# Performance work log

Measured on AMD Instinct MI355X. Metric: run time of the kernel, lower is better.

## Reference

```python
import jax, jax.numpy as jnp
import numpy as np

N = 30000      # nodes
NNZ = 480000   # edges (avg degree 16)
D_IN, D_H, D_OUT = 64, 256, 128


def spmm(rows, cols, vals, feat, n):
    # (sparse [n,n] in COO) @ feat : out[r] += vals[e] * feat[cols[e]]
    return jax.ops.segment_sum(vals[:, None] * feat[cols], rows, num_segments=n)


def graph_inception(l_feat, r_feat, rows, cols, vals, W1, b1, W2, b2):
    # hop=1, eval mode (F.dropout with training=False is identity)
    n = l_feat.shape[0]
    x0 = r_feat  # dropout(Korder_list[r][0])
    x1 = l_feat  # dropout(Korder_list[l][0])
    # network_l @ x0 and network_r (=transpose) @ x1
    l_K = spmm(rows, cols, vals, x0, n)          # [N, D]
    r_K = spmm(cols, rows, vals, x1, n)          # [N, D]
    l_re = l_K @ W1 + b1                          # weight1(l_Korder)
    r_re = r_K @ W1 + b1
    # Multiply: mm(network, a) * b then weight2 (mm result equals l_K / r_K)
    l_mul = (l_K * x1) @ W2 + b2
    r_mul = (r_K * x0) @ W2 + b2
    return l_re + l_mul, r_re + r_mul


def setup_inputs() -> dict:
    key = jax.random.key(0)
    ks = jax.random.split(key, 9)
    l_feat = jax.random.normal(ks[0], (N, D_IN), jnp.float32)
    r_feat = jax.random.normal(ks[1], (N, D_IN), jnp.float32)
    edge_rows = jax.random.randint(ks[2], (NNZ,), 0, N, jnp.int32)
    edge_cols = jax.random.randint(ks[3], (NNZ,), 0, N, jnp.int32)
    edge_vals = jax.random.uniform(ks[4], (NNZ,), jnp.float32)
    W1 = jax.random.normal(ks[5], (D_IN, D_H), jnp.float32) / np.sqrt(D_IN)
    W2 = jax.random.normal(ks[6], (D_IN, D_H), jnp.float32) / np.sqrt(D_IN)
    W3 = jax.random.normal(ks[7], (D_H, D_OUT), jnp.float32) / np.sqrt(D_H)
    W4 = jax.random.normal(ks[8], (D_H, D_OUT), jnp.float32) / np.sqrt(D_H)
    return {
        "l_feat": l_feat, "r_feat": r_feat,
        "edge_rows": edge_rows, "edge_cols": edge_cols, "edge_vals": edge_vals,
        "W1": W1, "b1": jnp.zeros((D_H,), jnp.float32),
        "W2": W2, "b2": jnp.zeros((D_H,), jnp.float32),
        "W3": W3, "b3": jnp.zeros((D_OUT,), jnp.float32),
        "W4": W4, "b4": jnp.zeros((D_OUT,), jnp.float32),
    }


def reference(l_feat, r_feat, edge_rows, edge_cols, edge_vals,
              W1, b1, W2, b2, W3, b3, W4, b4):
    a1, b1_ = graph_inception(l_feat, r_feat, edge_rows, edge_cols, edge_vals, W1, b1, W2, b2)
    y1 = jax.nn.relu(a1)
    z1 = jax.nn.relu(b1_)
    a2, _ = graph_inception(y1, z1, edge_rows, edge_cols, edge_vals, W3, b3, W4, b4)
    return jax.nn.relu(a2)  # [N, 128]
```

## Files before the change

kernel.cpp:

```cpp
#include <hip/hip_runtime.h>

#define NN     30000
#define NNZE   480000
#define NPART  8
#define PROWS  (NN / NPART)
#define NCHUNK 32
#define CH_E   (NNZE / NCHUNK)
#define HBIN   (NN / 2)
#define SCB    118

using s8 = __attribute__((ext_vector_type(8))) short;
using f4 = __attribute__((ext_vector_type(4))) float;

__device__ __forceinline__ unsigned short f2bf(float x) {
    unsigned int u = __float_as_uint(x);
    u += 0x7fff + ((u >> 16) & 1);
    return (unsigned short)(u >> 16);
}
__device__ __forceinline__ float bf2f(unsigned short h) {
    return __uint_as_float(((unsigned int)h) << 16);
}
__device__ __forceinline__ float bflo(unsigned int z) {
    return __uint_as_float(z << 16);
}
__device__ __forceinline__ float bfhi(unsigned int z) {
    return __uint_as_float(z & 0xffff0000u);
}
__device__ __forceinline__ int2 nt_pair(const int2* p) {
    long long v = __builtin_nontemporal_load((const long long*)p);
    int2 r; r.x = (int)(unsigned int)v; r.y = (int)(v >> 32); return r;
}

#define FEAT4   (NN * 64 / 4)
#define PREP_W0 (2 * FEAT4)
#define PREP_W1 (PREP_W0 + 98688)
__global__ __launch_bounds__(256) void prep_kernel(
    const float* __restrict__ lf, const float* __restrict__ rf,
    const float* __restrict__ W1, const float* __restrict__ W2,
    const float* __restrict__ W3, const float* __restrict__ W4,
    const float* __restrict__ b1, const float* __restrict__ b2,
    const float* __restrict__ b3, const float* __restrict__ b4,
    unsigned short* __restrict__ lfb, unsigned short* __restrict__ rfb,
    unsigned short* __restrict__ Wt1, unsigned short* __restrict__ Wt2,
    float* __restrict__ bias1, float* __restrict__ bias2)
{
    int i = blockIdx.x * 256 + threadIdx.x;
    if (i < PREP_W0) {
        const float* src = (i < FEAT4) ? lf : rf;
        unsigned short* dst = (i < FEAT4) ? lfb : rfb;
        int j = (i < FEAT4) ? i : i - FEAT4;
        float4 v = ((const float4*)src)[j];
        ushort4 o;
        o.x = f2bf(v.x); o.y = f2bf(v.y); o.z = f2bf(v.z); o.w = f2bf(v.w);
        ((ushort4*)dst)[j] = o;
    } else if (i < PREP_W1) {
        int j = i - PREP_W0;
        if (j < 32768) {
            int n = j >> 7, k = j & 127;
            float v = (k < 64) ? W1[(size_t)k * 256 + n] : W2[(size_t)(k - 64) * 256 + n];
            Wt1[j] = f2bf(v);
        } else if (j < 32768 + 65536) {
            int q = j - 32768;
            int n = q >> 9, k = q & 511;
            float v = (k < 256) ? W3[(size_t)k * 128 + n] : W4[(size_t)(k - 256) * 128 + n];
            Wt2[q] = f2bf(v);
        } else if (j < 98304 + 256) {
            int n = j - 98304; bias1[n] = b1[n] + b2[n];
        } else if (j < 98560 + 128) {
            int n = j - 98560; bias2[n] = b3[n] + b4[n];
        }
    }
}

__global__ __launch_bounds__(256) void count_rank_kernel(
    const int* __restrict__ rows, const int* __restrict__ cols,
    int* __restrict__ histP,
    unsigned short* __restrict__ rank_r, unsigned short* __restrict__ rank_c)
{
    int b = blockIdx.x;
    int side  = b >> 6;
    int chunk = (b & 63) >> 1;
    int half  = b & 1;
    const int* keys = side ? cols : rows;
    unsigned short* rank = side ? rank_c : rank_r;
    int binlo = half * HBIN;

    __shared__ int h[HBIN];
    for (int i = threadIdx.x; i < HBIN; i += 256) h[i] = 0;
    __syncthreads();

    int e0 = chunk * CH_E;
    for (int e = e0 + threadIdx.x; e < e0 + CH_E; e += 256) {
        int k = __builtin_nontemporal_load(keys + e) - binlo;
        if ((unsigned)k < (unsigned)HBIN)
            rank[e] = (unsigned short)atomicAdd(&h[k], 1);
    }
    __syncthreads();

    int* dst = histP + ((size_t)(side * NCHUNK + chunk)) * NN + binlo;
    for (int i = threadIdx.x; i < HBIN; i += 256)
        __builtin_nontemporal_store(h[i], dst + i);
}

__global__ __launch_bounds__(256) void scanP_kernel(
    int* __restrict__ histP,
    int* __restrict__ rp, int* __restrict__ cp, int* __restrict__ totals)
{
    int b = blockIdx.x;
    int side = (b >= SCB) ? 1 : 0;
    int lb = side ? b - SCB : b;
    int t = threadIdx.x;
    int bin = lb * 256 + t;

    int run = 0;
    if (bin < NN) {
        int* base = histP + (size_t)side * NCHUNK * NN + bin;
#pragma unroll 4
        for (int c = 0; c < NCHUNK; ++c) {
            int v = base[(size_t)c * NN];
            base[(size_t)c * NN] = run;
            run += v;
        }
    }
    __shared__ int s[256];
    s[t] = run;
    __syncthreads();
#pragma unroll
    for (int off = 1; off < 256; off <<= 1) {
        int u = (t >= off) ? s[t - off] : 0;
        __syncthreads();
        s[t] += u;
        __syncthreads();
    }
    if (bin < NN) (side ? cp : rp)[bin] = s[t] - run;
    if (t == 255) totals[b] = s[t];
}

__global__ __launch_bounds__(256) void scan_addtot_kernel(
    int* __restrict__ rp, int* __restrict__ cp, const int* __restrict__ totals)
{
    int b = blockIdx.x;
    int side = (b >= SCB) ? 1 : 0;
    int lb = side ? b - SCB : b;
    int t = threadIdx.x;

    __shared__ int s[128];
    if (t < 128) s[t] = (t < SCB) ? totals[side * SCB + t] : 0;
    __syncthreads();
#pragma unroll
    for (int off = 1; off < 128; off <<= 1) {
        int u = 0;
        if (t < 128 && t >= off) u = s[t - off];
        __syncthreads();
        if (t < 128) s[t] += u;
        __syncthreads();
    }
    int off = (lb == 0) ? 0 : s[lb - 1];
    int idx = lb * 256 + t;
    int* ptr = side ? cp : rp;
    if (idx < NN) ptr[idx] += off;
    if (b == 0   && t == 0) rp[NN] = NNZE;
    if (b == SCB && t == 0) cp[NN] = NNZE;
}

__global__ __launch_bounds__(256) void scatter_rank_kernel(
    const int* __restrict__ rows, const int* __restrict__ cols,
    const float* __restrict__ vals,
    const unsigned short* __restrict__ rank_r, const unsigned short* __restrict__ rank_c,
    const int* __restrict__ histP,
    const int* __restrict__ rp, const int* __restrict__ cp,
    int2* __restrict__ csr_pair, int2* __restrict__ csc_pair)
{
    int part = blockIdx.x & (NPART - 1);
    int lo = part * PROWS, hi = lo + PROWS;
    int nb = gridDim.x >> 3;
    int bj = blockIdx.x >> 3;
    int stride = nb * 256;
    for (int e = bj * 256 + threadIdx.x; e < NNZE; e += stride) {
        int r = __builtin_nontemporal_load(rows + e);
        int c = __builtin_nontemporal_load(cols + e);
        float fv = __builtin_nontemporal_load(vals + e);
        int vb = __float_as_int(fv);
        int chunk = e / CH_E;
        if (r >= lo && r < hi) {
            int p = rp[r] + histP[(size_t)chunk * NN + r]
                  + (int)__builtin_nontemporal_load(rank_r + e);
            csr_pair[p] = make_int2(c, vb);
        }
        if (c >= lo && c < hi) {
            int q = cp[c] + histP[(size_t)(NCHUNK + chunk) * NN + c]
                  + (int)__builtin_nontemporal_load(rank_c + e);
            csc_pair[q] = make_int2(r, vb);
        }
    }
}

__global__ __launch_bounds__(256) void gather64_x_kernel(
    const int* __restrict__ rp, const int2* __restrict__ rpair,
    const int* __restrict__ cp, const int2* __restrict__ cpair,
    const unsigned short* __restrict__ lfb, const unsigned short* __restrict__ rfb,
    unsigned short* __restrict__ X1, unsigned short* __restrict__ X2)
{
    int side = blockIdx.y;
    const int*  ptr  = side ? cp    : rp;
    const int2* pair = side ? cpair : rpair;
    const unsigned int* gf = (const unsigned int*)(side ? lfb : rfb);
    const unsigned int* mf = (const unsigned int*)(side ? rfb : lfb);
    unsigned int* X = (unsigned int*)(side ? X2 : X1);

    int w = blockIdx.x * 8 + (threadIdx.x >> 5);
    int l = threadIdx.x & 31;
    int e0 = ptr[w], e1 = ptr[w + 1];
    float a0 = 0.f, a1 = 0.f;
    int e = e0;
    for (; e + 7 < e1; e += 8) {
        int2 p[8];
#pragma unroll
        for (int j = 0; j < 8; ++j) p[j] = nt_pair(&pair[e + j]);
        unsigned int z[8];
#pragma unroll
        for (int j = 0; j < 8; ++j) z[j] = gf[(size_t)p[j].x * 32 + l];
#pragma unroll
        for (int j = 0; j < 8; ++j) {
            float v = __int_as_float(p[j].y);
            a0 += v * bflo(z[j]);
            a1 += v * bfhi(z[j]);
        }
    }
    for (; e < e1; ++e) {
        int2 p0 = nt_pair(&pair[e]);
        unsigned int z0 = gf[(size_t)p0.x * 32 + l];
        float v = __int_as_float(p0.y);
        a0 += v * bflo(z0);
        a1 += v * bfhi(z0);
    }
    unsigned int m = mf[(size_t)w * 32 + l];
    float m0 = a0 * bflo(m);
    float m1 = a1 * bfhi(m);
    X[(size_t)w * 64 + l]      = (unsigned int)f2bf(a0) | ((unsigned int)f2bf(a1) << 16);
    X[(size_t)w * 64 + 32 + l] = (unsigned int)f2bf(m0) | ((unsigned int)f2bf(m1) << 16);
}

__global__ __launch_bounds__(256) void gather256_x_kernel(
    const int* __restrict__ ptr, const int2* __restrict__ pair,
    const unsigned short* __restrict__ z1b, const unsigned short* __restrict__ y1b,
    unsigned short* __restrict__ X3)
{
    int w    = blockIdx.x * 4 + (threadIdx.x >> 6);
    int lane = threadIdx.x & 63;
    int e0 = ptr[w], e1 = ptr[w + 1];
    const ushort4* Z = (const ushort4*)z1b;
    f4 acc = {0.f, 0.f, 0.f, 0.f};
    int e = e0;
    for (; e + 7 < e1; e += 8) {
        int2 p[8];
#pragma unroll
        for (int j = 0; j < 8; ++j) p[j] = nt_pair(&pair[e + j]);
        ushort4 z[8];
#pragma unroll
        for (int j = 0; j < 8; ++j) z[j] = Z[(size_t)p[j].x * 64 + lane];
#pragma unroll
        for (int j = 0; j < 8; ++j) {
            float v = __int_as_float(p[j].y);
            acc[0] += v * bf2f(z[j].x);
            acc[1] += v * bf2f(z[j].y);
            acc[2] += v * bf2f(z[j].z);
            acc[3] += v * bf2f(z[j].w);
        }
    }
    for (; e < e1; ++e) {
        int2 p0 = nt_pair(&pair[e]);
        float v0 = __int_as_float(p0.y);
        ushort4 z0 = Z[(size_t)p0.x * 64 + lane];
        acc[0] += v0 * bf2f(z0.x);
        acc[1] += v0 * bf2f(z0.y);
        acc[2] += v0 * bf2f(z0.z);
        acc[3] += v0 * bf2f(z0.w);
    }
    ushort4 y = ((const ushort4*)y1b)[(size_t)w * 64 + lane];
    ushort4 o0, o1;
    o0.x = f2bf(acc[0]); o0.y = f2bf(acc[1]); o0.z = f2bf(acc[2]); o0.w = f2bf(acc[3]);
    o1.x = f2bf(acc[0] * bf2f(y.x));
    o1.y = f2bf(acc[1] * bf2f(y.y));
    o1.z = f2bf(acc[2] * bf2f(y.z));
    o1.w = f2bf(acc[3] * bf2f(y.w));
    ((ushort4*)X3)[(size_t)w * 128 + lane]      = o0;
    ((ushort4*)X3)[(size_t)w * 128 + 64 + lane] = o1;
}

template<int K, int DOUT, bool OUT_BF16>
__global__ __launch_bounds__(256) void mfma_gemm_kernel(
    const unsigned short* Xa, const unsigned short* Xb,
    const unsigned short* __restrict__ Wt, const float* __restrict__ bias,
    void* outa, void* outb)
{
    constexpr int WC = DOUT / 4;
    constexpr int FN = WC / 16;
    __shared__ s8 sX[64 * 8];
    __shared__ s8 sW[DOUT * 8];

    const unsigned short* X = blockIdx.y ? Xb : Xa;
    void* outv              = blockIdx.y ? outb : outa;

    const int t       = threadIdx.x;
    const int rowbase = blockIdx.x * 64;
    const int wid     = t >> 6;
    const int lane    = t & 63;
    const int l15     = lane & 15;
    const int kg      = lane >> 4;

    f4 acc[4][FN] = {};

    for (int kc = 0; kc < K; kc += 64) {
#pragma unroll
        for (int it = 0; it < 2; ++it) {
            int ch = t + it * 256;
            int r = ch >> 3, c = ch & 7;
            int row = rowbase + r;
            s8 v = {};
            if (row < NN) v = ((const s8*)X)[((size_t)row * K + kc) / 8 + c];
            sX[(r << 3) | (c ^ (r & 7))] = v;
        }
#pragma unroll
        for (int it = 0; it < DOUT / 32; ++it) {
            int ch = t + it * 256;
            int n = ch >> 3, c = ch & 7;
            sW[(n << 3) | (c ^ (n & 7))] = ((const s8*)Wt)[((size_t)n * K + kc) / 8 + c];
        }
        __syncthreads();

#pragma unroll
        for (int ks = 0; ks < 2; ++ks) {
            int cch = ks * 4 + kg;
            s8 a[4], b[FN];
#pragma unroll
            for (int fm = 0; fm < 4; ++fm) {
                int r0 = fm * 16 + l15;
                a[fm] = sX[(r0 << 3) | (cch ^ (r0 & 7))];
            }
#pragma unroll
            for (int fn = 0; fn < FN; ++fn) {
                int n0 = wid * WC + fn * 16 + l15;
                b[fn] = sW[(n0 << 3) | (cch ^ (n0 & 7))];
            }
#pragma unroll
            for (int fm = 0; fm < 4; ++fm)
#pragma unroll
                for (int fn = 0; fn < FN; ++fn)
                    acc[fm][fn] = __builtin_amdgcn_mfma_f32_16x16x32_bf16(
                        a[fm], b[fn], acc[fm][fn], 0, 0, 0);
        }
        __syncthreads();
    }

#pragma unroll
    for (int fm = 0; fm < 4; ++fm) {
#pragma unroll
        for (int fn = 0; fn < FN; ++fn) {
            int col = wid * WC + fn * 16 + l15;
            float bv = bias[col];
#pragma unroll
            for (int j = 0; j < 4; ++j) {
                int row = rowbase + fm * 16 + kg * 4 + j;
                if (row < NN) {
                    float v = fmaxf(acc[fm][fn][j] + bv, 0.f);
                    if constexpr (OUT_BF16)
                        ((unsigned short*)outv)[(size_t)row * DOUT + col] = f2bf(v);
                    else
                        ((float*)outv)[(size_t)row * DOUT + col] = v;
                }
            }
        }
    }
}

extern "C" void kernel_launch(void* const* d_in, const int* in_sizes, int n_in,
                              void* d_out, int out_size, void* d_ws, size_t ws_size,
                              hipStream_t stream)
{
    const float* l_feat = (const float*)d_in[0];
    const float* r_feat = (const float*)d_in[1];
    const int*   rows   = (const int*)  d_in[2];
    const int*   cols   = (const int*)  d_in[3];
    const float* vals   = (const float*)d_in[4];
    const float* W1     = (const float*)d_in[5];
    const float* b1     = (const float*)d_in[6];
    const float* W2     = (const float*)d_in[7];
    const float* b2     = (const float*)d_in[8];
    const float* W3     = (const float*)d_in[9];
    const float* b3     = (const float*)d_in[10];
    const float* W4     = (const float*)d_in[11];
    const float* b4     = (const float*)d_in[12];
    float* out = (float*)d_out;

    char* p = (char*)d_ws;
    unsigned short* X1  = (unsigned short*)p; p += (size_t)NN * 128 * 2;
    unsigned short* X2  = (unsigned short*)p; p += (size_t)NN * 128 * 2;
    unsigned short* X3  = (unsigned short*)p; p += (size_t)NN * 512 * 2;
    unsigned short* z1b = (unsigned short*)p; p += (size_t)NN * 256 * 2;
    unsigned short* y1b = (unsigned short*)p; p += (size_t)NN * 256 * 2;
    unsigned short* lfb = (unsigned short*)p; p += (size_t)NN * 64 * 2;
    unsigned short* rfb = (unsigned short*)p; p += (size_t)NN * 64 * 2;
    int* histP    = (int*)p; p += (size_t)2 * NCHUNK * NN * 4;
    int* totals   = (int*)p; p += 256 * 4;
    unsigned short* Wt1 = (unsigned short*)p; p += 32768 * 2;
    unsigned short* Wt2 = (unsigned short*)p; p += 65536 * 2;
    float* bias1 = (float*)p; p += 256 * 4;
    float* bias2 = (float*)p; p += 128 * 4;
    int*   row_ptr  = (int*)p; p += (size_t)(NN + 4) * 4;
    int*   col_ptr  = (int*)p; p += (size_t)(NN + 4) * 4;
    int2*  csr_pair = (int2*)p; p += (size_t)NNZE * 8;
    int2*  csc_pair = (int2*)p; p += (size_t)NNZE * 8;
    unsigned short* rank_r = (unsigned short*)p; p += (size_t)NNZE * 2;
    unsigned short* rank_c = (unsigned short*)p; p += (size_t)NNZE * 2;

    prep_kernel<<<(PREP_W1 + 255) / 256, 256, 0, stream>>>(
        l_feat, r_feat, W1, W2, W3, W4, b1, b2, b3, b4,
        lfb, rfb, Wt1, Wt2, bias1, bias2);

    count_rank_kernel<<<128, 256, 0, stream>>>(rows, cols, histP, rank_r, rank_c);

    scanP_kernel<<<2 * SCB, 256, 0, stream>>>(histP, row_ptr, col_ptr, totals);
    scan_addtot_kernel<<<2 * SCB, 256, 0, stream>>>(row_ptr, col_ptr, totals);

    scatter_rank_kernel<<<1024, 256, 0, stream>>>(
        rows, cols, vals, rank_r, rank_c, histP, row_ptr, col_ptr, csr_pair, csc_pair);

    {
        dim3 grid(NN / 8, 2);
        gather64_x_kernel<<<grid, 256, 0, stream>>>(
            row_ptr, csr_pair, col_ptr, csc_pair, lfb, rfb, X1, X2);
    }

    {
        dim3 grid((NN + 63) / 64, 2);
        mfma_gemm_kernel<128, 256, true><<<grid, 256, 0, stream>>>(
            X1, X2, Wt1, bias1, y1b, z1b);
    }

    gather256_x_kernel<<<NN / 4, 256, 0, stream>>>(row_ptr, csr_pair, z1b, y1b, X3);

    {
        dim3 grid((NN + 63) / 64, 1);
        mfma_gemm_kernel<512, 128, false><<<grid, 256, 0, stream>>>(
            X3, X3, Wt2, bias2, out, out);
    }
}
```

Before: 198.5 us.

## Stage edge pairs in LDS per block and use nontemporal loads/stores in gathers and GEMMs

Each gather block now loads its whole contiguous edge-pair range into shared memory cooperatively before per-row accumulation, so rows read their pairs from LDS instead of each warp issuing its own global loads. If a block's range exceeds the LDS capacity, the remaining pairs fall back to global loads. The gather64 unroll drops from 8 to 4. Nontemporal loads and stores are added for the gather outputs, for GEMM input tiles, and selectively for GEMM outputs, so streaming data does not evict the feature tables used by the random gathers. The trade-off is an added block-wide sync and less memory-level parallelism in gather64.

Result: no change. 199.4 us (+0.5%).

```diff
diff --git a/kernel.cpp b/kernel.cpp
--- a/kernel.cpp
+++ b/kernel.cpp
@@ -29,6 +29,9 @@
 __device__ __forceinline__ int2 nt_pair(const int2* p) {
     long long v = __builtin_nontemporal_load((const long long*)p);
     int2 r; r.x = (int)(unsigned int)v; r.y = (int)(v >> 32); return r;
+}
+__device__ __forceinline__ unsigned long long nt_u64(const void* p) {
+    return __builtin_nontemporal_load((const unsigned long long*)p);
 }
 
 #define FEAT4   (NN * 64 / 4)
@@ -195,6 +198,7 @@
     }
 }
 
+#define G64CAP 768
 __global__ __launch_bounds__(256) void gather64_x_kernel(
     const int* __restrict__ rp, const int2* __restrict__ rpair,
     const int* __restrict__ cp, const int2* __restrict__ cpair,
@@ -208,27 +212,36 @@
     const unsigned int* mf = (const unsigned int*)(side ? rfb : lfb);
     unsigned int* X = (unsigned int*)(side ? X2 : X1);
 
-    int w = blockIdx.x * 8 + (threadIdx.x >> 5);
+    __shared__ int2 sp[G64CAP];
+    int w0 = blockIdx.x * 8;
+    int e0b = ptr[w0];
+    int nseg = ptr[w0 + 8] - e0b;
+    for (int i = threadIdx.x; i < nseg && i < G64CAP; i += 256)
+        sp[i] = nt_pair(&pair[e0b + i]);
+    __syncthreads();
+
+    int w = w0 + (threadIdx.x >> 5);
     int l = threadIdx.x & 31;
-    int e0 = ptr[w], e1 = ptr[w + 1];
+    int ea = ptr[w] - e0b, eb = ptr[w + 1] - e0b;
     float a0 = 0.f, a1 = 0.f;
-    int e = e0;
-    for (; e + 7 < e1; e += 8) {
-        int2 p[8];
-#pragma unroll
-        for (int j = 0; j < 8; ++j) p[j] = nt_pair(&pair[e + j]);
-        unsigned int z[8];
-#pragma unroll
-        for (int j = 0; j < 8; ++j) z[j] = gf[(size_t)p[j].x * 32 + l];
-#pragma unroll
-        for (int j = 0; j < 8; ++j) {
+    int e = ea;
+    for (; e + 3 < eb; e += 4) {
+        int2 p[4];
+#pragma unroll
+        for (int j = 0; j < 4; ++j)
+            p[j] = (e + j < G64CAP) ? sp[e + j] : nt_pair(&pair[e0b + e + j]);
+        unsigned int z[4];
+#pragma unroll
+        for (int j = 0; j < 4; ++j) z[j] = gf[(size_t)p[j].x * 32 + l];
+#pragma unroll
+        for (int j = 0; j < 4; ++j) {
             float v = __int_as_float(p[j].y);
             a0 += v * bflo(z[j]);
             a1 += v * bfhi(z[j]);
         }
     }
-    for (; e < e1; ++e) {
-        int2 p0 = nt_pair(&pair[e]);
+    for (; e < eb; ++e) {
+        int2 p0 = (e < G64CAP) ? sp[e] : nt_pair(&pair[e0b + e]);
         unsigned int z0 = gf[(size_t)p0.x * 32 + l];
         float v = __int_as_float(p0.y);
         a0 += v * bflo(z0);
@@ -237,25 +250,37 @@
     unsigned int m = mf[(size_t)w * 32 + l];
     float m0 = a0 * bflo(m);
     float m1 = a1 * bfhi(m);
-    X[(size_t)w * 64 + l]      = (unsigned int)f2bf(a0) | ((unsigned int)f2bf(a1) << 16);
-    X[(size_t)w * 64 + 32 + l] = (unsigned int)f2bf(m0) | ((unsigned int)f2bf(m1) << 16);
-}
-
+    unsigned int o0 = (unsigned int)f2bf(a0) | ((unsigned int)f2bf(a1) << 16);
+    unsigned int o1 = (unsigned int)f2bf(m0) | ((unsigned int)f2bf(m1) << 16);
+    __builtin_nontemporal_store(o0, &X[(size_t)w * 64 + l]);
+    __builtin_nontemporal_store(o1, &X[(size_t)w * 64 + 32 + l]);
+}
+
+#define G256CAP 512
 __global__ __launch_bounds__(256) void gather256_x_kernel(
     const int* __restrict__ ptr, const int2* __restrict__ pair,
     const unsigned short* __restrict__ z1b, const unsigned short* __restrict__ y1b,
     unsigned short* __restrict__ X3)
 {
-    int w    = blockIdx.x * 4 + (threadIdx.x >> 6);
+    __shared__ int2 sp[G256CAP];
+    int w0 = blockIdx.x * 4;
+    int e0b = ptr[w0];
+    int nseg = ptr[w0 + 4] - e0b;
+    for (int i = threadIdx.x; i < nseg && i < G256CAP; i += 256)
+        sp[i] = nt_pair(&pair[e0b + i]);
+    __syncthreads();
+
+    int w    = w0 + (threadIdx.x >> 6);
     int lane = threadIdx.x & 63;
-    int e0 = ptr[w], e1 = ptr[w + 1];
+    int ea = ptr[w] - e0b, eb = ptr[w + 1] - e0b;
     const ushort4* Z = (const ushort4*)z1b;
     f4 acc = {0.f, 0.f, 0.f, 0.f};
-    int e = e0;
-    for (; e + 7 < e1; e += 8) {
+    int e = ea;
+    for (; e + 7 < eb; e += 8) {
         int2 p[8];
 #pragma unroll
-        for (int j = 0; j < 8; ++j) p[j] = nt_pair(&pair[e + j]);
+        for (int j = 0; j < 8; ++j)
+            p[j] = (e + j < G256CAP) ? sp[e + j] : nt_pair(&pair[e0b + e + j]);
         ushort4 z[8];
 #pragma unroll
         for (int j = 0; j < 8; ++j) z[j] = Z[(size_t)p[j].x * 64 + lane];
@@ -268,8 +293,8 @@
             acc[3] += v * bf2f(z[j].w);
         }
     }
-    for (; e < e1; ++e) {
-        int2 p0 = nt_pair(&pair[e]);
+    for (; e < eb; ++e) {
+        int2 p0 = (e < G256CAP) ? sp[e] : nt_pair(&pair[e0b + e]);
         float v0 = __int_as_float(p0.y);
         ushort4 z0 = Z[(size_t)p0.x * 64 + lane];
         acc[0] += v0 * bf2f(z0.x);
@@ -277,18 +302,27 @@
         acc[2] += v0 * bf2f(z0.z);
         acc[3] += v0 * bf2f(z0.w);
     }
-    ushort4 y = ((const ushort4*)y1b)[(size_t)w * 64 + lane];
-    ushort4 o0, o1;
-    o0.x = f2bf(acc[0]); o0.y = f2bf(acc[1]); o0.z = f2bf(acc[2]); o0.w = f2bf(acc[3]);
-    o1.x = f2bf(acc[0] * bf2f(y.x));
-    o1.y = f2bf(acc[1] * bf2f(y.y));
-    o1.z = f2bf(acc[2] * bf2f(y.z));
-    o1.w = f2bf(acc[3] * bf2f(y.w));
-    ((ushort4*)X3)[(size_t)w * 128 + lane]      = o0;
-    ((ushort4*)X3)[(size_t)w * 128 + 64 + lane] = o1;
-}
-
-template<int K, int DOUT, bool OUT_BF16>
+    unsigned long long yu = nt_u64(&((const ushort4*)y1b)[(size_t)w * 64 + lane]);
+    float y0 = bf2f((unsigned short)(yu));
+    float y1 = bf2f((unsigned short)(yu >> 16));
+    float y2 = bf2f((unsigned short)(yu >> 32));
+    float y3 = bf2f((unsigned short)(yu >> 48));
+    unsigned long long o0 =
+        (unsigned long long)f2bf(acc[0])
+      | ((unsigned long long)f2bf(acc[1]) << 16)
+      | ((unsigned long long)f2bf(acc[2]) << 32)
+      | ((unsigned long long)f2bf(acc[3]) << 48);
+    unsigned long long o1 =
+        (unsigned long long)f2bf(acc[0] * y0)
+      | ((unsigned long long)f2bf(acc[1] * y1) << 16)
+      | ((unsigned long long)f2bf(acc[2] * y2) << 32)
+      | ((unsigned long long)f2bf(acc[3] * y3) << 48);
+    unsigned long long* X3u = (unsigned long long*)X3;
+    __builtin_nontemporal_store(o0, &X3u[(size_t)w * 128 + lane]);
+    __builtin_nontemporal_store(o1, &X3u[(size_t)w * 128 + 64 + lane]);
+}
+
+template<int K, int DOUT, bool OUT_BF16, bool NT_A, bool NT_B>
 __global__ __launch_bounds__(256) void mfma_gemm_kernel(
     const unsigned short* Xa, const unsigned short* Xb,
     const unsigned short* __restrict__ Wt, const float* __restrict__ bias,
@@ -301,6 +335,7 @@
 
     const unsigned short* X = blockIdx.y ? Xb : Xa;
     void* outv              = blockIdx.y ? outb : outa;
+    const bool nt_out       = blockIdx.y ? NT_B : NT_A;
 
     const int t       = threadIdx.x;
     const int rowbase = blockIdx.x * 64;
@@ -318,7 +353,8 @@
             int r = ch >> 3, c = ch & 7;
             int row = rowbase + r;
             s8 v = {};
-            if (row < NN) v = ((const s8*)X)[((size_t)row * K + kc) / 8 + c];
+            if (row < NN)
+                v = __builtin_nontemporal_load(((const s8*)X) + ((size_t)row * K + kc) / 8 + c);
             sX[(r << 3) | (c ^ (r & 7))] = v;
         }
 #pragma unroll
@@ -364,10 +400,15 @@
                 int row = rowbase + fm * 16 + kg * 4 + j;
                 if (row < NN) {
                     float v = fmaxf(acc[fm][fn][j] + bv, 0.f);
-                    if constexpr (OUT_BF16)
-                        ((unsigned short*)outv)[(size_t)row * DOUT + col] = f2bf(v);
-                    else
-                        ((float*)outv)[(size_t)row * DOUT + col] = v;
+                    if constexpr (OUT_BF16) {
+                        unsigned short* q = (unsigned short*)outv + (size_t)row * DOUT + col;
+                        if (nt_out) __builtin_nontemporal_store(f2bf(v), q);
+                        else        *q = f2bf(v);
+                    } else {
+                        float* q = (float*)outv + (size_t)row * DOUT + col;
+                        if (nt_out) __builtin_nontemporal_store(v, q);
+                        else        *q = v;
+                    }
                 }
             }
         }
@@ -434,7 +475,7 @@
 
     {
         dim3 grid((NN + 63) / 64, 2);
-        mfma_gemm_kernel<128, 256, true><<<grid, 256, 0, stream>>>(
+        mfma_gemm_kernel<128, 256, true, true, false><<<grid, 256, 0, stream>>>(
             X1, X2, Wt1, bias1, y1b, z1b);
     }
 
@@ -442,7 +483,7 @@
 
     {
         dim3 grid((NN + 63) / 64, 1);
-        mfma_gemm_kernel<512, 128, false><<<grid, 256, 0, stream>>>(
+        mfma_gemm_kernel<512, 128, false, true, true><<<grid, 256, 0, stream>>>(
             X3, X3, Wt2, bias2, out, out);
     }
 }
```

## Fuse SpMM gathers with following MFMA GEMMs via shared-memory staging

Applied to the files above, without the earlier changes.

Merges each sparse gather kernel with the dense MFMA GEMM that follows it. The gathered row block (32 rows) is written to swizzled LDS and multiplied directly, so the X1/X2/X3 intermediate buffers are no longer written to and re-read from global memory. Layer-1 and layer-2 outputs also use nontemporal stores where they are not reread. The trade-off is smaller 32-row GEMM tiles that reload the weights per block, and less gather parallelism per block, which may reduce latency hiding.

After: 236.2 us. 1.19x slower.

```diff
diff --git a/kernel.cpp b/kernel.cpp
--- a/kernel.cpp
+++ b/kernel.cpp
@@ -29,6 +29,9 @@
 __device__ __forceinline__ int2 nt_pair(const int2* p) {
     long long v = __builtin_nontemporal_load((const long long*)p);
     int2 r; r.x = (int)(unsigned int)v; r.y = (int)(v >> 32); return r;
+}
+__device__ __forceinline__ unsigned long long nt_u64(const void* p) {
+    return __builtin_nontemporal_load((const unsigned long long*)p);
 }
 
 #define FEAT4   (NN * 64 / 4)
@@ -195,179 +198,252 @@
     }
 }
 
-__global__ __launch_bounds__(256) void gather64_x_kernel(
+__global__ __launch_bounds__(256) void fused_l1_kernel(
     const int* __restrict__ rp, const int2* __restrict__ rpair,
     const int* __restrict__ cp, const int2* __restrict__ cpair,
     const unsigned short* __restrict__ lfb, const unsigned short* __restrict__ rfb,
-    unsigned short* __restrict__ X1, unsigned short* __restrict__ X2)
-{
+    const unsigned short* __restrict__ Wt1, const float* __restrict__ bias1,
+    unsigned short* __restrict__ y1b, unsigned short* __restrict__ z1b)
+{
+    __shared__ s8 sX[32 * 16];
+    __shared__ s8 sW[256 * 8];
+    unsigned int* sXu = (unsigned int*)sX;
+
     int side = blockIdx.y;
     const int*  ptr  = side ? cp    : rp;
     const int2* pair = side ? cpair : rpair;
     const unsigned int* gf = (const unsigned int*)(side ? lfb : rfb);
     const unsigned int* mf = (const unsigned int*)(side ? rfb : lfb);
-    unsigned int* X = (unsigned int*)(side ? X2 : X1);
-
-    int w = blockIdx.x * 8 + (threadIdx.x >> 5);
-    int l = threadIdx.x & 31;
-    int e0 = ptr[w], e1 = ptr[w + 1];
-    float a0 = 0.f, a1 = 0.f;
-    int e = e0;
-    for (; e + 7 < e1; e += 8) {
-        int2 p[8];
-#pragma unroll
-        for (int j = 0; j < 8; ++j) p[j] = nt_pair(&pair[e + j]);
-        unsigned int z[8];
-#pragma unroll
-        for (int j = 0; j < 8; ++j) z[j] = gf[(size_t)p[j].x * 32 + l];
-#pragma unroll
-        for (int j = 0; j < 8; ++j) {
-            float v = __int_as_float(p[j].y);
-            a0 += v * bflo(z[j]);
-            a1 += v * bfhi(z[j]);
-        }
-    }
-    for (; e < e1; ++e) {
-        int2 p0 = nt_pair(&pair[e]);
-        unsigned int z0 = gf[(size_t)p0.x * 32 + l];
-        float v = __int_as_float(p0.y);
-        a0 += v * bflo(z0);
-        a1 += v * bfhi(z0);
-    }
-    unsigned int m = mf[(size_t)w * 32 + l];
-    float m0 = a0 * bflo(m);
-    float m1 = a1 * bfhi(m);
-    X[(size_t)w * 64 + l]      = (unsigned int)f2bf(a0) | ((unsigned int)f2bf(a1) << 16);
-    X[(size_t)w * 64 + 32 + l] = (unsigned int)f2bf(m0) | ((unsigned int)f2bf(m1) << 16);
-}
-
-__global__ __launch_bounds__(256) void gather256_x_kernel(
+    unsigned short* outp   = side ? z1b : y1b;
+
+    const int t = threadIdx.x;
+    const int rowbase = blockIdx.x * 32;
+
+    int hw = t >> 5;
+    int l  = t & 31;
+#pragma unroll
+    for (int ri = 0; ri < 4; ++ri) {
+        int rl = ri * 8 + hw;
+        int w = rowbase + rl;
+        float a0 = 0.f, a1 = 0.f;
+        unsigned int m = 0;
+        if (w < NN) {
+            int e0 = ptr[w], e1 = ptr[w + 1];
+            int e = e0;
+            for (; e + 3 < e1; e += 4) {
+                int2 p[4];
+#pragma unroll
+                for (int j = 0; j < 4; ++j) p[j] = nt_pair(&pair[e + j]);
+                unsigned int z[4];
+#pragma unroll
+                for (int j = 0; j < 4; ++j) z[j] = gf[(size_t)p[j].x * 32 + l];
+#pragma unroll
+                for (int j = 0; j < 4; ++j) {
+                    float v = __int_as_float(p[j].y);
+                    a0 += v * bflo(z[j]);
+                    a1 += v * bfhi(z[j]);
+                }
+            }
+            for (; e < e1; ++e) {
+                int2 p0 = nt_pair(&pair[e]);
+                unsigned int z0 = gf[(size_t)p0.x * 32 + l];
+                float v = __int_as_float(p0.y);
+                a0 += v * bflo(z0);
+                a1 += v * bfhi(z0);
+            }
+            m = mf[(size_t)w * 32 + l];
+        }
+        float m0 = a0 * bflo(m);
+        float m1 = a1 * bfhi(m);
+        unsigned int o0 = (unsigned int)f2bf(a0) | ((unsigned int)f2bf(a1) << 16);
+        unsigned int o1 = (unsigned int)f2bf(m0) | ((unsigned int)f2bf(m1) << 16);
+        int sw0 = (l >> 2) ^ (rl & 7);
+        sXu[(((rl << 4) | sw0) << 2) | (l & 3)]       = o0;
+        sXu[(((rl << 4) | 8 | sw0) << 2) | (l & 3)]   = o1;
+    }
+    __syncthreads();
+
+    const int wid = t >> 6;
+    const int lane = t & 63;
+    const int l15 = lane & 15;
+    const int kg = lane >> 4;
+
+    f4 acc[2][4] = {};
+#pragma unroll
+    for (int kc = 0; kc < 2; ++kc) {
+        if (kc) __syncthreads();
+#pragma unroll
+        for (int it = 0; it < 8; ++it) {
+            int ch = t + it * 256;
+            int n = ch >> 3, c = ch & 7;
+            sW[(n << 3) | (c ^ (n & 7))] = ((const s8*)Wt1)[n * 16 + kc * 8 + c];
+        }
+        __syncthreads();
+#pragma unroll
+        for (int ks = 0; ks < 2; ++ks) {
+            int cch = ks * 4 + kg;
+            s8 a[2], b[4];
+#pragma unroll
+            for (int fm = 0; fm < 2; ++fm) {
+                int r0 = fm * 16 + l15;
+                a[fm] = sX[(r0 << 4) | (kc * 8) | (cch ^ (r0 & 7))];
+            }
+#pragma unroll
+            for (int fn = 0; fn < 4; ++fn) {
+                int n0 = wid * 64 + fn * 16 + l15;
+                b[fn] = sW[(n0 << 3) | (cch ^ (n0 & 7))];
+            }
+#pragma unroll
+            for (int fm = 0; fm < 2; ++fm)
+#pragma unroll
+                for (int fn = 0; fn < 4; ++fn)
+                    acc[fm][fn] = __builtin_amdgcn_mfma_f32_16x16x32_bf16(
+                        a[fm], b[fn], acc[fm][fn], 0, 0, 0);
+        }
+    }
+
+#pragma unroll
+    for (int fm = 0; fm < 2; ++fm) {
+#pragma unroll
+        for (int fn = 0; fn < 4; ++fn) {
+            int col = wid * 64 + fn * 16 + l15;
+            float bv = bias1[col];
+#pragma unroll
+            for (int j = 0; j < 4; ++j) {
+                int row = rowbase + fm * 16 + kg * 4 + j;
+                if (row < NN) {
+                    unsigned short hv = f2bf(fmaxf(acc[fm][fn][j] + bv, 0.f));
+                    unsigned short* q = outp + (size_t)row * 256 + col;
+                    if (side == 0) __builtin_nontemporal_store(hv, q);
+                    else           *q = hv;
+                }
+            }
+        }
+    }
+}
+
+__global__ __launch_bounds__(256) void fused_l2_kernel(
     const int* __restrict__ ptr, const int2* __restrict__ pair,
     const unsigned short* __restrict__ z1b, const unsigned short* __restrict__ y1b,
-    unsigned short* __restrict__ X3)
-{
-    int w    = blockIdx.x * 4 + (threadIdx.x >> 6);
-    int lane = threadIdx.x & 63;
-    int e0 = ptr[w], e1 = ptr[w + 1];
+    const unsigned short* __restrict__ Wt2, const float* __restrict__ bias2,
+    float* __restrict__ out)
+{
+    __shared__ s8 sX[32 * 64];
+    __shared__ s8 sW[128 * 8];
+    unsigned long long* sXu = (unsigned long long*)sX;
+
+    const int t = threadIdx.x;
+    const int rowbase = blockIdx.x * 32;
+    const int wid = t >> 6;
+    const int lane = t & 63;
+
     const ushort4* Z = (const ushort4*)z1b;
-    f4 acc = {0.f, 0.f, 0.f, 0.f};
-    int e = e0;
-    for (; e + 7 < e1; e += 8) {
-        int2 p[8];
-#pragma unroll
-        for (int j = 0; j < 8; ++j) p[j] = nt_pair(&pair[e + j]);
-        ushort4 z[8];
-#pragma unroll
-        for (int j = 0; j < 8; ++j) z[j] = Z[(size_t)p[j].x * 64 + lane];
-#pragma unroll
-        for (int j = 0; j < 8; ++j) {
-            float v = __int_as_float(p[j].y);
-            acc[0] += v * bf2f(z[j].x);
-            acc[1] += v * bf2f(z[j].y);
-            acc[2] += v * bf2f(z[j].z);
-            acc[3] += v * bf2f(z[j].w);
-        }
-    }
-    for (; e < e1; ++e) {
-        int2 p0 = nt_pair(&pair[e]);
-        float v0 = __int_as_float(p0.y);
-        ushort4 z0 = Z[(size_t)p0.x * 64 + lane];
-        acc[0] += v0 * bf2f(z0.x);
-        acc[1] += v0 * bf2f(z0.y);
-        acc[2] += v0 * bf2f(z0.z);
-        acc[3] += v0 * bf2f(z0.w);
-    }
-    ushort4 y = ((const ushort4*)y1b)[(size_t)w * 64 + lane];
-    ushort4 o0, o1;
-    o0.x = f2bf(acc[0]); o0.y = f2bf(acc[1]); o0.z = f2bf(acc[2]); o0.w = f2bf(acc[3]);
-    o1.x = f2bf(acc[0] * bf2f(y.x));
-    o1.y = f2bf(acc[1] * bf2f(y.y));
-    o1.z = f2bf(acc[2] * bf2f(y.z));
-    o1.w = f2bf(acc[3] * bf2f(y.w));
-    ((ushort4*)X3)[(size_t)w * 128 + lane]      = o0;
-    ((ushort4*)X3)[(size_t)w * 128 + 64 + lane] = o1;
-}
-
-template<int K, int DOUT, bool OUT_BF16>
-__global__ __launch_bounds__(256) void mfma_gemm_kernel(
-    const unsigned short* Xa, const unsigned short* Xb,
-    const unsigned short* __restrict__ Wt, const float* __restrict__ bias,
-    void* outa, void* outb)
-{
-    constexpr int WC = DOUT / 4;
-    constexpr int FN = WC / 16;
-    __shared__ s8 sX[64 * 8];
-    __shared__ s8 sW[DOUT * 8];
-
-    const unsigned short* X = blockIdx.y ? Xb : Xa;
-    void* outv              = blockIdx.y ? outb : outa;
-
-    const int t       = threadIdx.x;
-    const int rowbase = blockIdx.x * 64;
-    const int wid     = t >> 6;
-    const int lane    = t & 63;
-    const int l15     = lane & 15;
-    const int kg      = lane >> 4;
-
-    f4 acc[4][FN] = {};
-
-    for (int kc = 0; kc < K; kc += 64) {
-#pragma unroll
-        for (int it = 0; it < 2; ++it) {
-            int ch = t + it * 256;
-            int r = ch >> 3, c = ch & 7;
-            int row = rowbase + r;
-            s8 v = {};
-            if (row < NN) v = ((const s8*)X)[((size_t)row * K + kc) / 8 + c];
-            sX[(r << 3) | (c ^ (r & 7))] = v;
-        }
-#pragma unroll
-        for (int it = 0; it < DOUT / 32; ++it) {
+#pragma unroll
+    for (int ri = 0; ri < 8; ++ri) {
+        int rl = ri * 4 + wid;
+        int w = rowbase + rl;
+        f4 acc = {0.f, 0.f, 0.f, 0.f};
+        unsigned long long yu = 0;
+        if (w < NN) {
+            int e0 = ptr[w], e1 = ptr[w + 1];
+            int e = e0;
+            for (; e + 7 < e1; e += 8) {
+                int2 p[8];
+#pragma unroll
+                for (int j = 0; j < 8; ++j) p[j] = nt_pair(&pair[e + j]);
+                ushort4 z[8];
+#pragma unroll
+                for (int j = 0; j < 8; ++j) z[j] = Z[(size_t)p[j].x * 64 + lane];
+#pragma unroll
+                for (int j = 0; j < 8; ++j) {
+                    float v = __int_as_float(p[j].y);
+                    acc[0] += v * bf2f(z[j].x);
+                    acc[1] += v * bf2f(z[j].y);
+                    acc[2] += v * bf2f(z[j].z);
+                    acc[3] += v * bf2f(z[j].w);
+                }
+            }
+            for (; e < e1; ++e) {
+                int2 p0 = nt_pair(&pair[e]);
+                float v0 = __int_as_float(p0.y);
+                ushort4 z0 = Z[(size_t)p0.x * 64 + lane];
+                acc[0] += v0 * bf2f(z0.x);
+                acc[1] += v0 * bf2f(z0.y);
+                acc[2] += v0 * bf2f(z0.z);
+                acc[3] += v0 * bf2f(z0.w);
+            }
+            yu = nt_u64(&((const ushort4*)y1b)[(size_t)w * 64 + lane]);
+        }
+        float y0 = bf2f((unsigned short)(yu));
+        float y1 = bf2f((unsigned short)(yu >> 16));
+        float y2 = bf2f((unsigned short)(yu >> 32));
+        float y3 = bf2f((unsigned short)(yu >> 48));
+        unsigned long long o0 =
+            (unsigned long long)f2bf(acc[0])
+          | ((unsigned long long)f2bf(acc[1]) << 16)
+          | ((unsigned long long)f2bf(acc[2]) << 32)
+          | ((unsigned long long)f2bf(acc[3]) << 48);
+        unsigned long long o1 =
+            (unsigned long long)f2bf(acc[0] * y0)
+          | ((unsigned long long)f2bf(acc[1] * y1) << 16)
+          | ((unsigned long long)f2bf(acc[2] * y2) << 32)
+          | ((unsigned long long)f2bf(acc[3] * y3) << 48);
+        int ch0 = lane >> 1;
+        int sw0 = (ch0 & ~7) | ((ch0 & 7) ^ (rl & 7));
+        sXu[(((rl << 6) | sw0) << 1) | (lane & 1)]        = o0;
+        sXu[(((rl << 6) | 32 | sw0) << 1) | (lane & 1)]   = o1;
+    }
+    __syncthreads();
+
+    const int l15 = lane & 15;
+    const int kg = lane >> 4;
+
+    f4 acc[2][2] = {};
+#pragma unroll
+    for (int kc = 0; kc < 8; ++kc) {
+        if (kc) __syncthreads();
+#pragma unroll
+        for (int it = 0; it < 4; ++it) {
             int ch = t + it * 256;
             int n = ch >> 3, c = ch & 7;
-            sW[(n << 3) | (c ^ (n & 7))] = ((const s8*)Wt)[((size_t)n * K + kc) / 8 + c];
+            sW[(n << 3) | (c ^ (n & 7))] = ((const s8*)Wt2)[n * 64 + kc * 8 + c];
         }
         __syncthreads();
-
 #pragma unroll
         for (int ks = 0; ks < 2; ++ks) {
             int cch = ks * 4 + kg;
-            s8 a[4], b[FN];
-#pragma unroll
-            for (int fm = 0; fm < 4; ++fm) {
+            s8 a[2], b[2];
+#pragma unroll
+            for (int fm = 0; fm < 2; ++fm) {
                 int r0 = fm * 16 + l15;
-                a[fm] = sX[(r0 << 3) | (cch ^ (r0 & 7))];
-            }
-#pragma unroll
-            for (int fn = 0; fn < FN; ++fn) {
-                int n0 = wid * WC + fn * 16 + l15;
+                a[fm] = sX[(r0 << 6) | (kc * 8) | (cch ^ (r0 & 7))];
+            }
+#pragma unroll
+            for (int fn = 0; fn < 2; ++fn) {
+                int n0 = wid * 32 + fn * 16 + l15;
                 b[fn] = sW[(n0 << 3) | (cch ^ (n0 & 7))];
             }
 #pragma unroll
-            for (int fm = 0; fm < 4; ++fm)
-#pragma unroll
-                for (int fn = 0; fn < FN; ++fn)
+            for (int fm = 0; fm < 2; ++fm)
+#pragma unroll
+                for (int fn = 0; fn < 2; ++fn)
                     acc[fm][fn] = __builtin_amdgcn_mfma_f32_16x16x32_bf16(
                         a[fm], b[fn], acc[fm][fn], 0, 0, 0);
         }
-        __syncthreads();
-    }
-
-#pragma unroll
-    for (int fm = 0; fm < 4; ++fm) {
-#pragma unroll
-        for (int fn = 0; fn < FN; ++fn) {
-            int col = wid * WC + fn * 16 + l15;
-            float bv = bias[col];
+    }
+
+#pragma unroll
+    for (int fm = 0; fm < 2; ++fm) {
+#pragma unroll
+        for (int fn = 0; fn < 2; ++fn) {
+            int col = wid * 32 + fn * 16 + l15;
+            float bv = bias2[col];
 #pragma unroll
             for (int j = 0; j < 4; ++j) {
                 int row = rowbase + fm * 16 + kg * 4 + j;
                 if (row < NN) {
                     float v = fmaxf(acc[fm][fn][j] + bv, 0.f);
-                    if constexpr (OUT_BF16)
-                        ((unsigned short*)outv)[(size_t)row * DOUT + col] = f2bf(v);
-                    else
-                        ((float*)outv)[(size_t)row * DOUT + col] = v;
+                    __builtin_nontemporal_store(v, out + (size_t)row * 128 + col);
                 }
             }
         }
@@ -394,9 +470,6 @@
     float* out = (float*)d_out;
 
     char* p = (char*)d_ws;
-    unsigned short* X1  = (unsigned short*)p; p += (size_t)NN * 128 * 2;
-    unsigned short* X2  = (unsigned short*)p; p += (size_t)NN * 128 * 2;
-    unsigned short* X3  = (unsigned short*)p; p += (size_t)NN * 512 * 2;
     unsigned short* z1b = (unsigned short*)p; p += (size_t)NN * 256 * 2;
     unsigned short* y1b = (unsigned short*)p; p += (size_t)NN * 256 * 2;
     unsigned short* lfb = (unsigned short*)p; p += (size_t)NN * 64 * 2;
@@ -427,22 +500,14 @@
         rows, cols, vals, rank_r, rank_c, histP, row_ptr, col_ptr, csr_pair, csc_pair);
 
     {
-        dim3 grid(NN / 8, 2);
-        gather64_x_kernel<<<grid, 256, 0, stream>>>(
-            row_ptr, csr_pair, col_ptr, csc_pair, lfb, rfb, X1, X2);
+        dim3 grid((NN + 31) / 32, 2);
+        fused_l1_kernel<<<grid, 256, 0, stream>>>(
+            row_ptr, csr_pair, col_ptr, csc_pair, lfb, rfb, Wt1, bias1, y1b, z1b);
     }
 
     {
-        dim3 grid((NN + 63) / 64, 2);
-        mfma_gemm_kernel<128, 256, true><<<grid, 256, 0, stream>>>(
-            X1, X2, Wt1, bias1, y1b, z1b);
-    }
-
-    gather256_x_kernel<<<NN / 4, 256, 0, stream>>>(row_ptr, csr_pair, z1b, y1b, X3);
-
-    {
-        dim3 grid((NN + 63) / 64, 1);
-        mfma_gemm_kernel<512, 128, false><<<grid, 256, 0, stream>>>(
-            X3, X3, Wt2, bias2, out, out);
-    }
-}
+        dim3 grid((NN + 31) / 32);
+        fused_l2_kernel<<<grid, 256, 0, stream>>>(
+            row_ptr, csr_pair, z1b, y1b, Wt2, bias2, out);
+    }
+}
```
